# Kernel optimization log

Hardware: AMD Instinct MI355X
Metric: run time of the kernel (lower is better)

The kernel has to match this reference:

```python
import jax, jax.numpy as jnp
import numpy as np

B, T, I, H = 512, 256, 7, 64


def setup_inputs() -> dict:
    key = jax.random.key(0)
    d = {
        "x": jax.random.normal(jax.random.fold_in(key, 0), (B, T, I), jnp.float32),
        "C": jnp.zeros((B, H, H), jnp.float32),
        "n": jnp.zeros((B, H, H), jnp.float32),
    }
    for j, nm in enumerate(["Wq", "Wk", "Wv", "Wi", "Wf", "Wo"]):
        d[nm] = jax.random.normal(jax.random.fold_in(key, j + 1), (H, I), jnp.float32)
        d["b" + nm[1]] = jnp.zeros((H,), jnp.float32)
    return d


def reference(x, C, n, Wq, Wk, Wv, Wi, Wf, Wo, bq, bk, bv, bi, bf, bo):
    # x: [B,T,I]; C,n: [B,H,H] matrix memory / normalizer state
    Hdim = Wq.shape[0]
    scale = 1.0 / jnp.sqrt(jnp.asarray(Hdim, x.dtype))
    q = jnp.einsum('bti,hi->bth', x, Wq) + bq
    k = scale * (jnp.einsum('bti,hi->bth', x, Wk) + bk)
    v = jnp.einsum('bti,hi->bth', x, Wv) + bv
    i = jnp.exp(jnp.einsum('bti,hi->bth', x, Wi) + bi)
    f = jax.nn.sigmoid(jnp.einsum('bti,hi->bth', x, Wf) + bf)
    o = jax.nn.sigmoid(jnp.einsum('bti,hi->bth', x, Wo) + bo)
    # time-major for scan: each gate [T,B,H]
    gates = tuple(jnp.swapaxes(g, 0, 1) for g in (q, k, v, i, f, o))

    def step(carry, g):
        C, n = carry                      # [B,H,H]
        qt, kt, vt, it, ft, ot = g        # [B,H]
        ik = it * kt                      # [B,H]
        # torch: C = f*C + i*outer(v,k)  -> C[r,c] = f[c]*C[r,c] + i[c]*v[r]*k[c]
        C = ft[:, None, :] * C + ik[:, None, :] * vt[:, :, None]
        # torch: n = f*n + i*k (broadcast over rows)
        n = ft[:, None, :] * n + ik[:, None, :]
        num = jnp.einsum('brc,bc->br', C, qt)          # C @ q
        den = jnp.einsum('brc,br->bc', n, qt)          # n.T @ q
        h = ot * jnp.tanh(num / jnp.maximum(den, 1.0))
        return (C, n), h

    (C, n), hs = jax.lax.scan(step, (C, n), gates)
    return jnp.swapaxes(hs, 0, 1), C, n  # h: [B,T,H]
```

## Files before the change

kernel.cpp:

```cpp
#include <hip/hip_runtime.h>
#include <math.h>

#define B_ 512
#define T_ 256
#define I_ 7
#define H_ 64
#define L_ 16
#define NCH_ (T_ / L_)
#define L2E 1.44269504089f
#define GUARD2 (-21.64f)

typedef short bf16x8 __attribute__((ext_vector_type(8)));
typedef short short4v __attribute__((ext_vector_type(4)));
typedef float f32x4 __attribute__((ext_vector_type(4)));

__device__ __forceinline__ unsigned short f2bf(float f) {
  unsigned u = __float_as_uint(f);
  u += 0x7fff + ((u >> 16) & 1);
  return (unsigned short)(u >> 16);
}
__device__ __forceinline__ float bf2f(unsigned short u) {
  return __uint_as_float(((unsigned)u) << 16);
}
__device__ __forceinline__ float ex2(float x) { return __builtin_amdgcn_exp2f(x); }
__device__ __forceinline__ float lg2(float x) { return __builtin_amdgcn_logf(x); }
__device__ __forceinline__ float logsig2(float a2) {
  return (a2 < GUARD2) ? a2 : -lg2(1.f + ex2(-a2));
}
__device__ __forceinline__ float sig2(float a2) {
  return __fdividef(1.f, 1.f + ex2(-a2));
}

#define PACK_V(C) do {                                                        \
  const float* xp_ = xb + (C) * (L_ * I_);                                    \
  unsigned short vv[8];                                                       \
  _Pragma("unroll") for (int tt = 0; tt < 8; ++tt) {                          \
    const int t = th0 + tt;                                                   \
    float vp = bP;                                                            \
    _Pragma("unroll") for (int jj = 0; jj < 7; ++jj)                          \
      vp = fmaf(xp_[t * 7 + jj], wP[jj], vp);                                 \
    vv[tt] = f2bf(vp);                                                        \
  }                                                                           \
  short4v p0 = {(short)vv[0], (short)vv[1], (short)vv[2], (short)vv[3]};      \
  short4v p1 = {(short)vv[4], (short)vv[5], (short)vv[6], (short)vv[7]};      \
  *(short4v*)&sVT[(C) & 1][lane][th0]     = p0;                               \
  *(short4v*)&sVT[(C) & 1][lane][th0 + 4] = p1;                               \
} while (0)

#define PACK_O(C) do {                                                        \
  const float* xp_ = xb + (C) * (L_ * I_);                                    \
  _Pragma("unroll") for (int tt = 0; tt < 8; ++tt) {                          \
    const int t = th0 + tt;                                                   \
    float op = bP;                                                            \
    _Pragma("unroll") for (int jj = 0; jj < 7; ++jj)                          \
      op = fmaf(xp_[t * 7 + jj], wP[jj], op);                                 \
    sOpre[(C) & 1][t][lane] = f2bf(op);                                       \
  }                                                                           \
} while (0)

#define IK_PRE(C) do {                                                        \
  const float* xp_ = xb + (C) * (L_ * I_);                                    \
  _Pragma("unroll") for (int tt = 0; tt < 8; ++tt) {                          \
    const int t = tb + tt;                                                    \
    float xs[7];                                                              \
    _Pragma("unroll") for (int jj = 0; jj < 7; ++jj) xs[jj] = xp_[t * 7 + jj];\
    float ip = bI2, kp = bK;                                                  \
    _Pragma("unroll") for (int jj = 0; jj < 7; ++jj) {                        \
      ip = fmaf(xs[jj], wi2[jj], ip);                                         \
      kp = fmaf(xs[jj], wk[jj], kp);                                          \
    }                                                                         \
    const float ik = ex2(ip) * kp * 0.125f;                                   \
    ik8[tt] = ik;                                                             \
    sIK[(C) & 1][t][lane] = ik;                                               \
  }                                                                           \
} while (0)

#define IK_EXP(C) do {                                                        \
  float cl[16];                                                               \
  _Pragma("unroll") for (int t = 0; t < 16; ++t) cl[t] = sLs[(C) & 1][lane][t]; \
  _Pragma("unroll") for (int t = 1; t < 16; ++t) cl[t] += cl[t - 1];          \
  const float m = cl[7];                                                      \
  const float scl = ex2(cl[15] - m);                                          \
  unsigned short kh[8];                                                       \
  _Pragma("unroll") for (int tt = 0; tt < 8; ++tt) {                          \
    const int t = tb + tt;                                                    \
    const float u = ik8[tt] * ex2(m - cl[t]);                                 \
    sKt[(C) & 1][t][lane] = f2bf(u);                                          \
    kh[tt] = f2bf(u * scl);                                                   \
  }                                                                           \
  short4v p0 = {(short)kh[0], (short)kh[1], (short)kh[2], (short)kh[3]};      \
  short4v p1 = {(short)kh[4], (short)kh[5], (short)kh[6], (short)kh[7]};      \
  *(short4v*)&sKnT[(C) & 1][lane][tb]     = p0;                               \
  *(short4v*)&sKnT[(C) & 1][lane][tb + 4] = p1;                               \
} while (0)

#define F_HALF(C) do {                                                        \
  const float* xp_ = xb + (C) * (L_ * I_);                                    \
  _Pragma("unroll") for (int tt = 0; tt < 8; ++tt) {                          \
    const int t = ftb + tt;                                                   \
    float fp = bF2;                                                           \
    _Pragma("unroll") for (int jj = 0; jj < 7; ++jj)                          \
      fp = fmaf(xp_[t * 7 + jj], wf2[jj], fp);                                \
    sLs[(C) & 1][lane][t] = logsig2(fp);                                      \
  }                                                                           \
} while (0)

#define SCALQ(C) do {                                                         \
  const float* xp_ = xb + (C) * (L_ * I_);                                    \
  float cl[16];                                                               \
  _Pragma("unroll") for (int t = 0; t < 16; ++t) cl[t] = sLs[(C) & 1][lane][t]; \
  _Pragma("unroll") for (int t = 1; t < 16; ++t) cl[t] += cl[t - 1];          \
  sEM[(C) & 1][lane]   = ex2(cl[7]);                                          \
  sFtot[(C) & 1][lane] = ex2(cl[15]);                                         \
  if (lane < 16) {                                                            \
    float Sqv = wqs[7];                                                       \
    _Pragma("unroll") for (int jj = 0; jj < 7; ++jj)                          \
      Sqv = fmaf(xp_[lane * 7 + jj], wqs[jj], Sqv);                           \
    sSq[(C) & 1][lane] = Sqv;                                                 \
  }                                                                           \
  const float m = cl[7];                                                      \
  _Pragma("unroll") for (int t = 0; t < 8; ++t) {                             \
    float qq = bQ;                                                            \
    _Pragma("unroll") for (int jj = 0; jj < 7; ++jj)                          \
      qq = fmaf(xp_[t * 7 + jj], wq[jj], qq);                                 \
    sQt[(C) & 1][t][lane] = f2bf(qq * ex2(cl[t] - m));                        \
  }                                                                           \
} while (0)

#define QDEN(C) do {                                                          \
  const float* xp_ = xb + (C) * (L_ * I_);                                    \
  float ls[16], cl[16];                                                       \
  _Pragma("unroll") for (int t = 0; t < 16; ++t) ls[t] = sLs[(C) & 1][lane][t]; \
  _Pragma("unroll") for (int t = 0; t < 16; ++t) {                            \
    nv = fmaf(ex2(ls[t]), nv, sIK[(C) & 1][t][lane]);                         \
    sDen[(C) & 1][t][lane] = nv;                                              \
  }                                                                           \
  cl[0] = ls[0];                                                              \
  _Pragma("unroll") for (int t = 1; t < 16; ++t) cl[t] = cl[t - 1] + ls[t];   \
  const float m = cl[7];                                                      \
  _Pragma("unroll") for (int t = 8; t < 16; ++t) {                            \
    float qq = bQ;                                                            \
    _Pragma("unroll") for (int jj = 0; jj < 7; ++jj)                          \
      qq = fmaf(xp_[t * 7 + jj], wq[jj], qq);                                 \
    sQt[(C) & 1][t][lane] = f2bf(qq * ex2(cl[t] - m));                        \
  }                                                                           \
} while (0)

__global__ __launch_bounds__(512, 4) void mlstm_bal(
    const float* __restrict__ x,
    const float* __restrict__ Cin,
    const float* __restrict__ nin,
    const float* __restrict__ Wq, const float* __restrict__ bq,
    const float* __restrict__ Wk, const float* __restrict__ bk,
    const float* __restrict__ Wv, const float* __restrict__ bv,
    const float* __restrict__ Wi, const float* __restrict__ bi,
    const float* __restrict__ Wf, const float* __restrict__ bf,
    const float* __restrict__ Wo, const float* __restrict__ bo,
    float* __restrict__ hout, float* __restrict__ Cout, float* __restrict__ nout)
{
  const int b    = blockIdx.x;
  const int tid  = threadIdx.x;
  const int lane = tid & 63;
  const int w    = __builtin_amdgcn_readfirstlane(tid >> 6);
  const int quad = lane >> 4;
  const int sl   = lane & 15;

  __shared__ __align__(16) unsigned short sQt[2][L_][72];
  __shared__ __align__(16) unsigned short sKt[2][L_][72];
  __shared__ __align__(16) unsigned short sKnT[2][H_][40];
  __shared__ __align__(16) unsigned short sVT[2][H_][40];
  __shared__ __align__(16) unsigned short sS[4][L_][32];
  __shared__ __align__(16) unsigned short sC0[H_][72];
  __shared__ __align__(16) unsigned short sOpre[2][L_][72];
  __shared__ float sDen[2][L_][68];
  __shared__ float sIK[2][L_][H_];
  __shared__ float sLs[2][H_][17];
  __shared__ float sSq[2][L_];
  __shared__ float sEM[2][H_];
  __shared__ float sFtot[2][H_];
  __shared__ float sNv[H_];

  for (int idx = tid; idx < 1024; idx += 512) {
    const int r = idx >> 3, d = idx & 7;
    ((unsigned*)sKnT)[r * 20 + 8 + d] = 0;
    ((unsigned*)sVT)[r * 20 + 8 + d]  = 0;
  }
  for (int idx = tid; idx < 1024; idx += 512) ((unsigned*)sS)[idx] = 0;

  const float* __restrict__ xb = x + (size_t)b * T_ * I_;

  if (w < 4) {
    const int c0  = 16 * w + sl;
    const int th0 = (w < 2) ? 0 : 8;
    float wP[7];
    float bP;
    if ((w & 1) == 0) {
#pragma unroll
      for (int jj = 0; jj < 7; ++jj) wP[jj] = Wv[lane * 7 + jj];
      bP = bv[lane];
    } else {
#pragma unroll
      for (int jj = 0; jj < 7; ++jj) wP[jj] = Wo[lane * 7 + jj] * L2E;
      bP = bo[lane] * L2E;
    }
    f32x4 Cacc[4];
#pragma unroll
    for (int ct = 0; ct < 4; ++ct)
#pragma unroll
      for (int reg = 0; reg < 4; ++reg)
        Cacc[ct][reg] =
            Cin[(size_t)b * H_ * H_ + (size_t)(16 * w + 4 * quad + reg) * H_ + 16 * ct + sl];
    if ((w & 1) == 0) PACK_V(0); else PACK_O(0);
    __syncthreads();
    __syncthreads();
    for (int j = 0; j < NCH_; ++j) {
      const int p = j & 1;
      const bf16x8 aQ0 = *(const bf16x8*)&sQt[p][sl][8 * quad];
      const bf16x8 aQ1 = *(const bf16x8*)&sQt[p][sl][32 + 8 * quad];
      const bf16x8 bK0 = *(const bf16x8*)&sKt[p][sl][8 * quad];
      const bf16x8 bK1 = *(const bf16x8*)&sKt[p][sl][32 + 8 * quad];
      f32x4 Sv = {0.f, 0.f, 0.f, 0.f};
      Sv = __builtin_amdgcn_mfma_f32_16x16x32_bf16(aQ0, bK0, Sv, 0, 0, 0);
      Sv = __builtin_amdgcn_mfma_f32_16x16x32_bf16(aQ1, bK1, Sv, 0, 0, 0);
#pragma unroll
      for (int reg = 0; reg < 4; ++reg) {
        const int t = 4 * quad + reg;
        sS[w][t][sl] = f2bf((sl <= t) ? Sv[reg] : 0.f);
      }
      const bf16x8 aV = *(const bf16x8*)&sVT[p][c0][8 * quad];
#pragma unroll
      for (int ct = 0; ct < 4; ++ct) {
        const int cc = 16 * ct + sl;
        const float em = sEM[p][cc];
        const float ft = sFtot[p][cc];
#pragma unroll
        for (int reg = 0; reg < 4; ++reg)
          sC0[16 * w + 4 * quad + reg][cc] = f2bf(Cacc[ct][reg] * em);
        Cacc[ct] *= ft;
        const bf16x8 bH = *(const bf16x8*)&sKnT[p][cc][8 * quad];
        Cacc[ct] = __builtin_amdgcn_mfma_f32_16x16x32_bf16(aV, bH, Cacc[ct], 0, 0, 0);
      }
      if (j + 1 < NCH_) { if ((w & 1) == 0) PACK_V(j + 1); else PACK_O(j + 1); }
      __syncthreads();
      const bf16x8 bC0a = *(const bf16x8*)&sC0[c0][8 * quad];
      const bf16x8 bC0b = *(const bf16x8*)&sC0[c0][32 + 8 * quad];
      const bf16x8 aS   = *(const bf16x8*)&sS[w][sl][8 * quad];
      f32x4 Num = {0.f, 0.f, 0.f, 0.f};
      Num = __builtin_amdgcn_mfma_f32_16x16x32_bf16(aQ0, bC0a, Num, 0, 0, 0);
      Num = __builtin_amdgcn_mfma_f32_16x16x32_bf16(aQ1, bC0b, Num, 0, 0, 0);
      Num = __builtin_amdgcn_mfma_f32_16x16x32_bf16(aS, aV, Num, 0, 0, 0);
#pragma unroll
      for (int reg = 0; reg < 4; ++reg) {
        const int t = 4 * quad + reg;
        const float den = sDen[p][t][c0];
        const float idn = __fdividef(1.f, fmaxf(den * sSq[p][t], 1.f));
        const float o   = sig2(bf2f(sOpre[p][t][c0]));
        const float y = Num[reg] * idn;
        const float e = ex2(y * 2.88539008178f);
        const float th = 1.f - __fdividef(2.f, e + 1.f);
        hout[(size_t)b * T_ * H_ + (size_t)(j * L_ + t) * H_ + c0] = o * th;
      }
      __syncthreads();
    }
#pragma unroll
    for (int ct = 0; ct < 4; ++ct)
#pragma unroll
      for (int reg = 0; reg < 4; ++reg)
        Cout[(size_t)b * H_ * H_ + (size_t)(16 * w + 4 * quad + reg) * H_ + 16 * ct + sl] =
            Cacc[ct][reg];
  } else if (w == 4 || w == 5) {
    const int tb = (w == 4) ? 0 : 8;
    float wi2[7], wk[7];
#pragma unroll
    for (int jj = 0; jj < 7; ++jj) {
      wi2[jj] = Wi[lane * 7 + jj] * L2E;
      wk[jj]  = Wk[lane * 7 + jj];
    }
    const float bI2 = bi[lane] * L2E, bK = bk[lane];
    float ik8[8];
    IK_PRE(0);
    __syncthreads();
    IK_EXP(0);
    __syncthreads();
    for (int j = 0; j < NCH_; ++j) {
      if (j + 1 < NCH_) IK_PRE(j + 1);
      __syncthreads();
      if (j + 1 < NCH_) IK_EXP(j + 1);
      __syncthreads();
    }
  } else if (w == 6) {
    const int ftb = 0;
    float wf2[7], wq[7], wqs[8];
#pragma unroll
    for (int jj = 0; jj < 7; ++jj) {
      wf2[jj] = Wf[lane * 7 + jj] * L2E;
      wq[jj]  = Wq[lane * 7 + jj];
    }
    const float bF2 = bf[lane] * L2E, bQ = bq[lane];
#pragma unroll
    for (int jj = 0; jj < 7; ++jj) {
      float s = wq[jj];
#pragma unroll
      for (int off = 32; off >= 1; off >>= 1) s += __shfl_xor(s, off);
      wqs[jj] = s;
    }
    {
      float s = bQ;
#pragma unroll
      for (int off = 32; off >= 1; off >>= 1) s += __shfl_xor(s, off);
      wqs[7] = s;
    }
    F_HALF(0);
    __syncthreads();
    SCALQ(0);
    __syncthreads();
    for (int j = 0; j < NCH_; ++j) {
      if (j + 1 < NCH_) F_HALF(j + 1);
      __syncthreads();
      if (j + 1 < NCH_) SCALQ(j + 1);
      __syncthreads();
    }
  } else {
    const int ftb = 8;
    float wf2[7], wq[7];
#pragma unroll
    for (int jj = 0; jj < 7; ++jj) {
      wf2[jj] = Wf[lane * 7 + jj] * L2E;
      wq[jj]  = Wq[lane * 7 + jj];
    }
    const float bF2 = bf[lane] * L2E, bQ = bq[lane];
    float nv = nin[(size_t)b * H_ * H_ + lane];
    F_HALF(0);
    __syncthreads();
    QDEN(0);
    __syncthreads();
    for (int j = 0; j < NCH_; ++j) {
      if (j + 1 < NCH_) F_HALF(j + 1);
      __syncthreads();
      if (j + 1 < NCH_) QDEN(j + 1);
      __syncthreads();
    }
    sNv[lane] = nv;
  }

  __syncthreads();
  {
    const float nvv = sNv[lane];
#pragma unroll
    for (int k = 0; k < 8; ++k)
      nout[(size_t)b * H_ * H_ + (size_t)(8 * w + k) * H_ + lane] = nvv;
  }
}

extern "C" void kernel_launch(void* const* d_in, const int* in_sizes, int n_in,
                              void* d_out, int out_size, void* d_ws, size_t ws_size,
                              hipStream_t stream) {
  const float* xp  = (const float*)d_in[0];
  const float* Cp  = (const float*)d_in[1];
  const float* np_ = (const float*)d_in[2];

  const float* W[6];
  const float* Bv[6];
  if (n_in >= 15 && in_sizes[4] == 64) {
    for (int g = 0; g < 6; ++g) {
      W[g]  = (const float*)d_in[3 + 2 * g];
      Bv[g] = (const float*)d_in[4 + 2 * g];
    }
  } else {
    for (int g = 0; g < 6; ++g) {
      W[g]  = (const float*)d_in[3 + g];
      Bv[g] = (const float*)d_in[9 + g];
    }
  }

  float* hout = (float*)d_out;
  float* Cout = hout + (size_t)B_ * T_ * H_;
  float* nout = Cout + (size_t)B_ * H_ * H_;

  mlstm_bal<<<dim3(B_), dim3(512), 0, stream>>>(
      xp, Cp, np_,
      W[0], Bv[0], W[1], Bv[1], W[2], Bv[2],
      W[3], Bv[3], W[4], Bv[4], W[5], Bv[5],
      hout, Cout, nout);
}
```

Before: 145.6 us.

## Double chunk length to 32 and redistribute gate and denominator work across waves

Chunk length grows from 16 to 32 timesteps, which halves the number of chunk iterations and block-wide barriers. The normalizer recurrence moves into the four compute waves, and the output gate is now computed inline from x instead of being staged in shared memory. Log-forget and i*k values are stored as bf16 to save LDS. The trade-off is more per-wave serial work (a 32-step nv recurrence in each compute wave), extra precision loss from bf16 cumulative log-sums, and heavier unrolled register use.

```diff
diff --git a/kernel.cpp b/kernel.cpp
--- a/kernel.cpp
+++ b/kernel.cpp
@@ -5,8 +5,8 @@
 #define T_ 256
 #define I_ 7
 #define H_ 64
-#define L_ 16
-#define NCH_ (T_ / L_)
+#define LC_ 32
+#define NC_ (T_ / LC_)
 #define L2E 1.44269504089f
 #define GUARD2 (-21.64f)
 
@@ -31,36 +31,25 @@
   return __fdividef(1.f, 1.f + ex2(-a2));
 }
 
-#define PACK_V(C) do {                                                        \
-  const float* xp_ = xb + (C) * (L_ * I_);                                    \
+#define PACK_V32(C) do {                                                      \
+  const float* xp_ = xb + (C) * (LC_ * I_);                                   \
   unsigned short vv[8];                                                       \
   _Pragma("unroll") for (int tt = 0; tt < 8; ++tt) {                          \
-    const int t = th0 + tt;                                                   \
-    float vp = bP;                                                            \
-    _Pragma("unroll") for (int jj = 0; jj < 7; ++jj)                          \
-      vp = fmaf(xp_[t * 7 + jj], wP[jj], vp);                                 \
+    const int t = vt0 + tt;                                                   \
+    float vp = bV;                                                            \
+    _Pragma("unroll") for (int jj = 0; jj < 7; ++jj)                          \
+      vp = fmaf(xp_[t * 7 + jj], wVl[jj], vp);                                \
     vv[tt] = f2bf(vp);                                                        \
   }                                                                           \
   short4v p0 = {(short)vv[0], (short)vv[1], (short)vv[2], (short)vv[3]};      \
   short4v p1 = {(short)vv[4], (short)vv[5], (short)vv[6], (short)vv[7]};      \
-  *(short4v*)&sVT[(C) & 1][lane][th0]     = p0;                               \
-  *(short4v*)&sVT[(C) & 1][lane][th0 + 4] = p1;                               \
-} while (0)
-
-#define PACK_O(C) do {                                                        \
-  const float* xp_ = xb + (C) * (L_ * I_);                                    \
-  _Pragma("unroll") for (int tt = 0; tt < 8; ++tt) {                          \
-    const int t = th0 + tt;                                                   \
-    float op = bP;                                                            \
-    _Pragma("unroll") for (int jj = 0; jj < 7; ++jj)                          \
-      op = fmaf(xp_[t * 7 + jj], wP[jj], op);                                 \
-    sOpre[(C) & 1][t][lane] = f2bf(op);                                       \
-  }                                                                           \
-} while (0)
-
-#define IK_PRE(C) do {                                                        \
-  const float* xp_ = xb + (C) * (L_ * I_);                                    \
-  _Pragma("unroll") for (int tt = 0; tt < 8; ++tt) {                          \
+  *(short4v*)&sVT[(C) & 1][lane][vt0]     = p0;                               \
+  *(short4v*)&sVT[(C) & 1][lane][vt0 + 4] = p1;                               \
+} while (0)
+
+#define IK_PRE32(C) do {                                                      \
+  const float* xp_ = xb + (C) * (LC_ * I_);                                   \
+  _Pragma("unroll") for (int tt = 0; tt < 16; ++tt) {                         \
     const int t = tb + tt;                                                    \
     float xs[7];                                                              \
     _Pragma("unroll") for (int jj = 0; jj < 7; ++jj) xs[jj] = xp_[t * 7 + jj];\
@@ -69,84 +58,82 @@
       ip = fmaf(xs[jj], wi2[jj], ip);                                         \
       kp = fmaf(xs[jj], wk[jj], kp);                                          \
     }                                                                         \
-    const float ik = ex2(ip) * kp * 0.125f;                                   \
-    ik8[tt] = ik;                                                             \
-    sIK[(C) & 1][t][lane] = ik;                                               \
-  }                                                                           \
-} while (0)
-
-#define IK_EXP(C) do {                                                        \
-  float cl[16];                                                               \
-  _Pragma("unroll") for (int t = 0; t < 16; ++t) cl[t] = sLs[(C) & 1][lane][t]; \
-  _Pragma("unroll") for (int t = 1; t < 16; ++t) cl[t] += cl[t - 1];          \
-  const float m = cl[7];                                                      \
-  const float scl = ex2(cl[15] - m);                                          \
-  unsigned short kh[8];                                                       \
-  _Pragma("unroll") for (int tt = 0; tt < 8; ++tt) {                          \
+    sIK[(C) & 1][t][lane] = f2bf(ex2(ip) * kp * 0.125f);                      \
+  }                                                                           \
+} while (0)
+
+#define IK_EXP32(C) do {                                                      \
+  float cl[32];                                                               \
+  _Pragma("unroll") for (int t = 0; t < 32; ++t)                              \
+    cl[t] = bf2f(sLs[(C) & 1][t][lane]);                                      \
+  _Pragma("unroll") for (int t = 1; t < 32; ++t) cl[t] += cl[t - 1];          \
+  const float m = cl[15];                                                     \
+  const float scl = ex2(cl[31] - m);                                          \
+  unsigned short kh[16];                                                      \
+  _Pragma("unroll") for (int tt = 0; tt < 16; ++tt) {                         \
     const int t = tb + tt;                                                    \
-    const float u = ik8[tt] * ex2(m - cl[t]);                                 \
+    const float ik = bf2f(sIK[(C) & 1][t][lane]);                             \
+    const float u = ik * ex2(m - cl[t]);                                      \
     sKt[(C) & 1][t][lane] = f2bf(u);                                          \
     kh[tt] = f2bf(u * scl);                                                   \
   }                                                                           \
-  short4v p0 = {(short)kh[0], (short)kh[1], (short)kh[2], (short)kh[3]};      \
-  short4v p1 = {(short)kh[4], (short)kh[5], (short)kh[6], (short)kh[7]};      \
-  *(short4v*)&sKnT[(C) & 1][lane][tb]     = p0;                               \
-  *(short4v*)&sKnT[(C) & 1][lane][tb + 4] = p1;                               \
-} while (0)
-
-#define F_HALF(C) do {                                                        \
-  const float* xp_ = xb + (C) * (L_ * I_);                                    \
-  _Pragma("unroll") for (int tt = 0; tt < 8; ++tt) {                          \
+  _Pragma("unroll") for (int g = 0; g < 4; ++g) {                             \
+    short4v pk = {(short)kh[4 * g], (short)kh[4 * g + 1],                     \
+                  (short)kh[4 * g + 2], (short)kh[4 * g + 3]};                \
+    *(short4v*)&sKnT[(C) & 1][lane][tb + 4 * g] = pk;                         \
+  }                                                                           \
+} while (0)
+
+#define F_HALF32(C) do {                                                      \
+  const float* xp_ = xb + (C) * (LC_ * I_);                                   \
+  _Pragma("unroll") for (int tt = 0; tt < 16; ++tt) {                         \
     const int t = ftb + tt;                                                   \
     float fp = bF2;                                                           \
     _Pragma("unroll") for (int jj = 0; jj < 7; ++jj)                          \
       fp = fmaf(xp_[t * 7 + jj], wf2[jj], fp);                                \
-    sLs[(C) & 1][lane][t] = logsig2(fp);                                      \
-  }                                                                           \
-} while (0)
-
-#define SCALQ(C) do {                                                         \
-  const float* xp_ = xb + (C) * (L_ * I_);                                    \
-  float cl[16];                                                               \
-  _Pragma("unroll") for (int t = 0; t < 16; ++t) cl[t] = sLs[(C) & 1][lane][t]; \
-  _Pragma("unroll") for (int t = 1; t < 16; ++t) cl[t] += cl[t - 1];          \
-  sEM[(C) & 1][lane]   = ex2(cl[7]);                                          \
-  sFtot[(C) & 1][lane] = ex2(cl[15]);                                         \
-  if (lane < 16) {                                                            \
+    sLs[(C) & 1][t][lane] = f2bf(logsig2(fp));                                \
+  }                                                                           \
+} while (0)
+
+#define SCALQ32(C) do {                                                       \
+  const float* xp_ = xb + (C) * (LC_ * I_);                                   \
+  float cl[32];                                                               \
+  _Pragma("unroll") for (int t = 0; t < 32; ++t)                              \
+    cl[t] = bf2f(sLs[(C) & 1][t][lane]);                                      \
+  _Pragma("unroll") for (int t = 1; t < 32; ++t) cl[t] += cl[t - 1];          \
+  const float m = cl[15];                                                     \
+  sEM[(C) & 1][lane]   = ex2(m);                                              \
+  sFtot[(C) & 1][lane] = ex2(cl[31]);                                         \
+  _Pragma("unroll") for (int t = 0; t < 16; ++t) {                            \
+    float qq = bQ;                                                            \
+    _Pragma("unroll") for (int jj = 0; jj < 7; ++jj)                          \
+      qq = fmaf(xp_[t * 7 + jj], wq[jj], qq);                                 \
+    sQt[(C) & 1][t][lane] = f2bf(qq * ex2(cl[t] - m));                        \
+  }                                                                           \
+} while (0)
+
+#define SQQ32(C) do {                                                         \
+  const float* xp_ = xb + (C) * (LC_ * I_);                                   \
+  float cl[32];                                                               \
+  _Pragma("unroll") for (int t = 0; t < 32; ++t)                              \
+    cl[t] = bf2f(sLs[(C) & 1][t][lane]);                                      \
+  _Pragma("unroll") for (int t = 1; t < 32; ++t) cl[t] += cl[t - 1];          \
+  const float m = cl[15];                                                     \
+  _Pragma("unroll") for (int t = 16; t < 32; ++t) {                           \
+    float qq = bQ;                                                            \
+    _Pragma("unroll") for (int jj = 0; jj < 7; ++jj)                          \
+      qq = fmaf(xp_[t * 7 + jj], wq[jj], qq);                                 \
+    sQt[(C) & 1][t][lane] = f2bf(qq * ex2(cl[t] - m));                        \
+  }                                                                           \
+  if (lane < 32) {                                                            \
     float Sqv = wqs[7];                                                       \
     _Pragma("unroll") for (int jj = 0; jj < 7; ++jj)                          \
       Sqv = fmaf(xp_[lane * 7 + jj], wqs[jj], Sqv);                           \
     sSq[(C) & 1][lane] = Sqv;                                                 \
   }                                                                           \
-  const float m = cl[7];                                                      \
-  _Pragma("unroll") for (int t = 0; t < 8; ++t) {                             \
-    float qq = bQ;                                                            \
-    _Pragma("unroll") for (int jj = 0; jj < 7; ++jj)                          \
-      qq = fmaf(xp_[t * 7 + jj], wq[jj], qq);                                 \
-    sQt[(C) & 1][t][lane] = f2bf(qq * ex2(cl[t] - m));                        \
-  }                                                                           \
-} while (0)
-
-#define QDEN(C) do {                                                          \
-  const float* xp_ = xb + (C) * (L_ * I_);                                    \
-  float ls[16], cl[16];                                                       \
-  _Pragma("unroll") for (int t = 0; t < 16; ++t) ls[t] = sLs[(C) & 1][lane][t]; \
-  _Pragma("unroll") for (int t = 0; t < 16; ++t) {                            \
-    nv = fmaf(ex2(ls[t]), nv, sIK[(C) & 1][t][lane]);                         \
-    sDen[(C) & 1][t][lane] = nv;                                              \
-  }                                                                           \
-  cl[0] = ls[0];                                                              \
-  _Pragma("unroll") for (int t = 1; t < 16; ++t) cl[t] = cl[t - 1] + ls[t];   \
-  const float m = cl[7];                                                      \
-  _Pragma("unroll") for (int t = 8; t < 16; ++t) {                            \
-    float qq = bQ;                                                            \
-    _Pragma("unroll") for (int jj = 0; jj < 7; ++jj)                          \
-      qq = fmaf(xp_[t * 7 + jj], wq[jj], qq);                                 \
-    sQt[(C) & 1][t][lane] = f2bf(qq * ex2(cl[t] - m));                        \
-  }                                                                           \
-} while (0)
-
-__global__ __launch_bounds__(512, 4) void mlstm_bal(
+} while (0)
+
+__global__ __launch_bounds__(512, 4) void mlstm32(
     const float* __restrict__ x,
     const float* __restrict__ Cin,
     const float* __restrict__ nin,
@@ -165,44 +152,33 @@
   const int quad = lane >> 4;
   const int sl   = lane & 15;
 
-  __shared__ __align__(16) unsigned short sQt[2][L_][72];
-  __shared__ __align__(16) unsigned short sKt[2][L_][72];
+  __shared__ __align__(16) unsigned short sQt[2][LC_][72];
+  __shared__ __align__(16) unsigned short sKt[2][LC_][72];
   __shared__ __align__(16) unsigned short sKnT[2][H_][40];
   __shared__ __align__(16) unsigned short sVT[2][H_][40];
-  __shared__ __align__(16) unsigned short sS[4][L_][32];
+  __shared__ __align__(16) unsigned short sS[LC_][40];
   __shared__ __align__(16) unsigned short sC0[H_][72];
-  __shared__ __align__(16) unsigned short sOpre[2][L_][72];
-  __shared__ float sDen[2][L_][68];
-  __shared__ float sIK[2][L_][H_];
-  __shared__ float sLs[2][H_][17];
-  __shared__ float sSq[2][L_];
+  __shared__ unsigned short sLs[2][LC_][66];
+  __shared__ unsigned short sIK[2][LC_][66];
+  __shared__ float sSq[2][LC_];
   __shared__ float sEM[2][H_];
   __shared__ float sFtot[2][H_];
   __shared__ float sNv[H_];
 
-  for (int idx = tid; idx < 1024; idx += 512) {
-    const int r = idx >> 3, d = idx & 7;
-    ((unsigned*)sKnT)[r * 20 + 8 + d] = 0;
-    ((unsigned*)sVT)[r * 20 + 8 + d]  = 0;
-  }
-  for (int idx = tid; idx < 1024; idx += 512) ((unsigned*)sS)[idx] = 0;
+  for (int idx = tid; idx < 640; idx += 512) ((unsigned*)sS)[idx] = 0;
 
   const float* __restrict__ xb = x + (size_t)b * T_ * I_;
 
   if (w < 4) {
     const int c0  = 16 * w + sl;
-    const int th0 = (w < 2) ? 0 : 8;
-    float wP[7];
-    float bP;
-    if ((w & 1) == 0) {
-#pragma unroll
-      for (int jj = 0; jj < 7; ++jj) wP[jj] = Wv[lane * 7 + jj];
-      bP = bv[lane];
-    } else {
-#pragma unroll
-      for (int jj = 0; jj < 7; ++jj) wP[jj] = Wo[lane * 7 + jj] * L2E;
-      bP = bo[lane] * L2E;
-    }
+    const int vt0 = 8 * w;
+    float wOl[7], wVl[7];
+#pragma unroll
+    for (int jj = 0; jj < 7; ++jj) {
+      wOl[jj] = Wo[c0 * 7 + jj] * L2E;
+      wVl[jj] = Wv[lane * 7 + jj];
+    }
+    const float bO2 = bo[c0] * L2E, bV = bv[lane];
     f32x4 Cacc[4];
 #pragma unroll
     for (int ct = 0; ct < 4; ++ct)
@@ -210,22 +186,36 @@
       for (int reg = 0; reg < 4; ++reg)
         Cacc[ct][reg] =
             Cin[(size_t)b * H_ * H_ + (size_t)(16 * w + 4 * quad + reg) * H_ + 16 * ct + sl];
-    if ((w & 1) == 0) PACK_V(0); else PACK_O(0);
-    __syncthreads();
-    __syncthreads();
-    for (int j = 0; j < NCH_; ++j) {
+    float nv = nin[(size_t)b * H_ * H_ + c0];
+    PACK_V32(0);
+    __syncthreads();
+    __syncthreads();
+    for (int j = 0; j < NC_; ++j) {
       const int p = j & 1;
-      const bf16x8 aQ0 = *(const bf16x8*)&sQt[p][sl][8 * quad];
-      const bf16x8 aQ1 = *(const bf16x8*)&sQt[p][sl][32 + 8 * quad];
-      const bf16x8 bK0 = *(const bf16x8*)&sKt[p][sl][8 * quad];
-      const bf16x8 bK1 = *(const bf16x8*)&sKt[p][sl][32 + 8 * quad];
-      f32x4 Sv = {0.f, 0.f, 0.f, 0.f};
-      Sv = __builtin_amdgcn_mfma_f32_16x16x32_bf16(aQ0, bK0, Sv, 0, 0, 0);
-      Sv = __builtin_amdgcn_mfma_f32_16x16x32_bf16(aQ1, bK1, Sv, 0, 0, 0);
-#pragma unroll
-      for (int reg = 0; reg < 4; ++reg) {
-        const int t = 4 * quad + reg;
-        sS[w][t][sl] = f2bf((sl <= t) ? Sv[reg] : 0.f);
+      const float* xc = xb + (size_t)j * LC_ * I_;
+      float den8[8];
+#pragma unroll
+      for (int t = 0; t < 32; ++t) {
+        const float fs = ex2(bf2f(sLs[p][t][c0]));
+        const float ik = bf2f(sIK[p][t][c0]);
+        nv = fmaf(fs, nv, ik);
+        if (((t >> 2) & 3) == quad) den8[((t >> 4) << 2) | (t & 3)] = nv;
+      }
+      if (w != 1) {
+        const int tt = w >> 1, ss2 = w & 1;
+        const bf16x8 aQ0 = *(const bf16x8*)&sQt[p][16 * tt + sl][8 * quad];
+        const bf16x8 aQ1 = *(const bf16x8*)&sQt[p][16 * tt + sl][32 + 8 * quad];
+        const bf16x8 bK0 = *(const bf16x8*)&sKt[p][16 * ss2 + sl][8 * quad];
+        const bf16x8 bK1 = *(const bf16x8*)&sKt[p][16 * ss2 + sl][32 + 8 * quad];
+        f32x4 Sv = {0.f, 0.f, 0.f, 0.f};
+        Sv = __builtin_amdgcn_mfma_f32_16x16x32_bf16(aQ0, bK0, Sv, 0, 0, 0);
+        Sv = __builtin_amdgcn_mfma_f32_16x16x32_bf16(aQ1, bK1, Sv, 0, 0, 0);
+#pragma unroll
+        for (int reg = 0; reg < 4; ++reg) {
+          const int t = 16 * tt + 4 * quad + reg;
+          const int s = 16 * ss2 + sl;
+          sS[t][s] = f2bf((s <= t) ? Sv[reg] : 0.f);
+        }
       }
       const bf16x8 aV = *(const bf16x8*)&sVT[p][c0][8 * quad];
 #pragma unroll
@@ -237,28 +227,36 @@
         for (int reg = 0; reg < 4; ++reg)
           sC0[16 * w + 4 * quad + reg][cc] = f2bf(Cacc[ct][reg] * em);
         Cacc[ct] *= ft;
-        const bf16x8 bH = *(const bf16x8*)&sKnT[p][cc][8 * quad];
-        Cacc[ct] = __builtin_amdgcn_mfma_f32_16x16x32_bf16(aV, bH, Cacc[ct], 0, 0, 0);
+        const bf16x8 bKn = *(const bf16x8*)&sKnT[p][cc][8 * quad];
+        Cacc[ct] = __builtin_amdgcn_mfma_f32_16x16x32_bf16(aV, bKn, Cacc[ct], 0, 0, 0);
       }
-      if (j + 1 < NCH_) { if ((w & 1) == 0) PACK_V(j + 1); else PACK_O(j + 1); }
+      if (j + 1 < NC_) PACK_V32(j + 1);
       __syncthreads();
       const bf16x8 bC0a = *(const bf16x8*)&sC0[c0][8 * quad];
       const bf16x8 bC0b = *(const bf16x8*)&sC0[c0][32 + 8 * quad];
-      const bf16x8 aS   = *(const bf16x8*)&sS[w][sl][8 * quad];
-      f32x4 Num = {0.f, 0.f, 0.f, 0.f};
-      Num = __builtin_amdgcn_mfma_f32_16x16x32_bf16(aQ0, bC0a, Num, 0, 0, 0);
-      Num = __builtin_amdgcn_mfma_f32_16x16x32_bf16(aQ1, bC0b, Num, 0, 0, 0);
-      Num = __builtin_amdgcn_mfma_f32_16x16x32_bf16(aS, aV, Num, 0, 0, 0);
-#pragma unroll
-      for (int reg = 0; reg < 4; ++reg) {
-        const int t = 4 * quad + reg;
-        const float den = sDen[p][t][c0];
-        const float idn = __fdividef(1.f, fmaxf(den * sSq[p][t], 1.f));
-        const float o   = sig2(bf2f(sOpre[p][t][c0]));
-        const float y = Num[reg] * idn;
-        const float e = ex2(y * 2.88539008178f);
-        const float th = 1.f - __fdividef(2.f, e + 1.f);
-        hout[(size_t)b * T_ * H_ + (size_t)(j * L_ + t) * H_ + c0] = o * th;
+#pragma unroll
+      for (int tt = 0; tt < 2; ++tt) {
+        const bf16x8 aQ0 = *(const bf16x8*)&sQt[p][16 * tt + sl][8 * quad];
+        const bf16x8 aQ1 = *(const bf16x8*)&sQt[p][16 * tt + sl][32 + 8 * quad];
+        const bf16x8 aS  = *(const bf16x8*)&sS[16 * tt + sl][8 * quad];
+        f32x4 Num = {0.f, 0.f, 0.f, 0.f};
+        Num = __builtin_amdgcn_mfma_f32_16x16x32_bf16(aQ0, bC0a, Num, 0, 0, 0);
+        Num = __builtin_amdgcn_mfma_f32_16x16x32_bf16(aQ1, bC0b, Num, 0, 0, 0);
+        Num = __builtin_amdgcn_mfma_f32_16x16x32_bf16(aS, aV, Num, 0, 0, 0);
+#pragma unroll
+        for (int reg = 0; reg < 4; ++reg) {
+          const int t = 16 * tt + 4 * quad + reg;
+          const float den = den8[tt * 4 + reg];
+          const float idn = __fdividef(1.f, fmaxf(den * sSq[p][t], 1.f));
+          float op = bO2;
+#pragma unroll
+          for (int jj = 0; jj < 7; ++jj) op = fmaf(xc[t * 7 + jj], wOl[jj], op);
+          const float o = sig2(op);
+          const float y = Num[reg] * idn;
+          const float e = ex2(y * 2.88539008178f);
+          const float th = 1.f - __fdividef(2.f, e + 1.f);
+          hout[(size_t)b * T_ * H_ + (size_t)(j * LC_ + t) * H_ + c0] = o * th;
+        }
       }
       __syncthreads();
     }
@@ -268,8 +266,9 @@
       for (int reg = 0; reg < 4; ++reg)
         Cout[(size_t)b * H_ * H_ + (size_t)(16 * w + 4 * quad + reg) * H_ + 16 * ct + sl] =
             Cacc[ct][reg];
+    if (quad == 0) sNv[c0] = nv;
   } else if (w == 4 || w == 5) {
-    const int tb = (w == 4) ? 0 : 8;
+    const int tb = (w == 4) ? 0 : 16;
     float wi2[7], wk[7];
 #pragma unroll
     for (int jj = 0; jj < 7; ++jj) {
@@ -277,26 +276,44 @@
       wk[jj]  = Wk[lane * 7 + jj];
     }
     const float bI2 = bi[lane] * L2E, bK = bk[lane];
-    float ik8[8];
-    IK_PRE(0);
-    __syncthreads();
-    IK_EXP(0);
-    __syncthreads();
-    for (int j = 0; j < NCH_; ++j) {
-      if (j + 1 < NCH_) IK_PRE(j + 1);
-      __syncthreads();
-      if (j + 1 < NCH_) IK_EXP(j + 1);
+    IK_PRE32(0);
+    __syncthreads();
+    IK_EXP32(0);
+    __syncthreads();
+    for (int j = 0; j < NC_; ++j) {
+      if (j + 1 < NC_) IK_PRE32(j + 1);
+      __syncthreads();
+      if (j + 1 < NC_) IK_EXP32(j + 1);
       __syncthreads();
     }
   } else if (w == 6) {
     const int ftb = 0;
-    float wf2[7], wq[7], wqs[8];
+    float wf2[7], wq[7];
 #pragma unroll
     for (int jj = 0; jj < 7; ++jj) {
       wf2[jj] = Wf[lane * 7 + jj] * L2E;
       wq[jj]  = Wq[lane * 7 + jj];
     }
     const float bF2 = bf[lane] * L2E, bQ = bq[lane];
+    F_HALF32(0);
+    __syncthreads();
+    SCALQ32(0);
+    __syncthreads();
+    for (int j = 0; j < NC_; ++j) {
+      if (j + 1 < NC_) F_HALF32(j + 1);
+      __syncthreads();
+      if (j + 1 < NC_) SCALQ32(j + 1);
+      __syncthreads();
+    }
+  } else {
+    const int ftb = 16;
+    float wf2[7], wq[7], wqs[8];
+#pragma unroll
+    for (int jj = 0; jj < 7; ++jj) {
+      wf2[jj] = Wf[lane * 7 + jj] * L2E;
+      wq[jj]  = Wq[lane * 7 + jj];
+    }
+    const float bF2 = bf[lane] * L2E, bQ = bq[lane];
 #pragma unroll
     for (int jj = 0; jj < 7; ++jj) {
       float s = wq[jj];
@@ -310,37 +327,16 @@
       for (int off = 32; off >= 1; off >>= 1) s += __shfl_xor(s, off);
       wqs[7] = s;
     }
-    F_HALF(0);
-    __syncthreads();
-    SCALQ(0);
-    __syncthreads();
-    for (int j = 0; j < NCH_; ++j) {
-      if (j + 1 < NCH_) F_HALF(j + 1);
-      __syncthreads();
-      if (j + 1 < NCH_) SCALQ(j + 1);
-      __syncthreads();
-    }
-  } else {
-    const int ftb = 8;
-    float wf2[7], wq[7];
-#pragma unroll
-    for (int jj = 0; jj < 7; ++jj) {
-      wf2[jj] = Wf[lane * 7 + jj] * L2E;
-      wq[jj]  = Wq[lane * 7 + jj];
-    }
-    const float bF2 = bf[lane] * L2E, bQ = bq[lane];
-    float nv = nin[(size_t)b * H_ * H_ + lane];
-    F_HALF(0);
-    __syncthreads();
-    QDEN(0);
-    __syncthreads();
-    for (int j = 0; j < NCH_; ++j) {
-      if (j + 1 < NCH_) F_HALF(j + 1);
-      __syncthreads();
-      if (j + 1 < NCH_) QDEN(j + 1);
-      __syncthreads();
-    }
-    sNv[lane] = nv;
+    F_HALF32(0);
+    __syncthreads();
+    SQQ32(0);
+    __syncthreads();
+    for (int j = 0; j < NC_; ++j) {
+      if (j + 1 < NC_) F_HALF32(j + 1);
+      __syncthreads();
+      if (j + 1 < NC_) SQQ32(j + 1);
+      __syncthreads();
+    }
   }
 
   __syncthreads();
@@ -377,7 +373,7 @@
   float* Cout = hout + (size_t)B_ * T_ * H_;
   float* nout = Cout + (size_t)B_ * H_ * H_;
 
-  mlstm_bal<<<dim3(B_), dim3(512), 0, stream>>>(
+  mlstm32<<<dim3(B_), dim3(512), 0, stream>>>(
       xp, Cp, np_,
       W[0], Bv[0], W[1], Bv[1], W[2], Bv[2],
       W[3], Bv[3], W[4], Bv[4], W[5], Bv[5],
```

Measured after the change: 168.0 us. +15.5%, slower.

## Offload V and O gate packing from MFMA waves to four dedicated waves

Applied to the files above, without the earlier changes.

The block grows from 8 to 12 waves. The V-gate and O-gate projection and packing, previously done by the four MFMA waves between their matrix-update and output phases, now run on four extra producer waves (two for V, two for O). This takes the packing work off the critical MFMA waves, so it overlaps with the recurrent C update and output computation. The cost is more threads per block, which may lower occupancy and register budget under the new launch bounds. Barrier counts are kept matched, with the V and O producer waves placing their pack calls at different barrier phases.

```diff
diff --git a/kernel.cpp b/kernel.cpp
--- a/kernel.cpp
+++ b/kernel.cpp
@@ -146,7 +146,7 @@
   }                                                                           \
 } while (0)
 
-__global__ __launch_bounds__(512, 4) void mlstm_bal(
+__global__ __launch_bounds__(768, 6) void mlstm_w12(
     const float* __restrict__ x,
     const float* __restrict__ Cin,
     const float* __restrict__ nin,
@@ -180,29 +180,17 @@
   __shared__ float sFtot[2][H_];
   __shared__ float sNv[H_];
 
-  for (int idx = tid; idx < 1024; idx += 512) {
+  for (int idx = tid; idx < 1024; idx += 768) {
     const int r = idx >> 3, d = idx & 7;
     ((unsigned*)sKnT)[r * 20 + 8 + d] = 0;
     ((unsigned*)sVT)[r * 20 + 8 + d]  = 0;
   }
-  for (int idx = tid; idx < 1024; idx += 512) ((unsigned*)sS)[idx] = 0;
+  for (int idx = tid; idx < 1024; idx += 768) ((unsigned*)sS)[idx] = 0;
 
   const float* __restrict__ xb = x + (size_t)b * T_ * I_;
 
   if (w < 4) {
-    const int c0  = 16 * w + sl;
-    const int th0 = (w < 2) ? 0 : 8;
-    float wP[7];
-    float bP;
-    if ((w & 1) == 0) {
-#pragma unroll
-      for (int jj = 0; jj < 7; ++jj) wP[jj] = Wv[lane * 7 + jj];
-      bP = bv[lane];
-    } else {
-#pragma unroll
-      for (int jj = 0; jj < 7; ++jj) wP[jj] = Wo[lane * 7 + jj] * L2E;
-      bP = bo[lane] * L2E;
-    }
+    const int c0 = 16 * w + sl;
     f32x4 Cacc[4];
 #pragma unroll
     for (int ct = 0; ct < 4; ++ct)
@@ -210,7 +198,6 @@
       for (int reg = 0; reg < 4; ++reg)
         Cacc[ct][reg] =
             Cin[(size_t)b * H_ * H_ + (size_t)(16 * w + 4 * quad + reg) * H_ + 16 * ct + sl];
-    if ((w & 1) == 0) PACK_V(0); else PACK_O(0);
     __syncthreads();
     __syncthreads();
     for (int j = 0; j < NCH_; ++j) {
@@ -240,7 +227,6 @@
         const bf16x8 bH = *(const bf16x8*)&sKnT[p][cc][8 * quad];
         Cacc[ct] = __builtin_amdgcn_mfma_f32_16x16x32_bf16(aV, bH, Cacc[ct], 0, 0, 0);
       }
-      if (j + 1 < NCH_) { if ((w & 1) == 0) PACK_V(j + 1); else PACK_O(j + 1); }
       __syncthreads();
       const bf16x8 bC0a = *(const bf16x8*)&sC0[c0][8 * quad];
       const bf16x8 bC0b = *(const bf16x8*)&sC0[c0][32 + 8 * quad];
@@ -320,7 +306,7 @@
       if (j + 1 < NCH_) SCALQ(j + 1);
       __syncthreads();
     }
-  } else {
+  } else if (w == 7) {
     const int ftb = 8;
     float wf2[7], wq[7];
 #pragma unroll
@@ -341,10 +327,38 @@
       __syncthreads();
     }
     sNv[lane] = nv;
+  } else if (w == 8 || w == 9) {
+    const int th0 = (w == 8) ? 0 : 8;
+    float wP[7];
+#pragma unroll
+    for (int jj = 0; jj < 7; ++jj) wP[jj] = Wv[lane * 7 + jj];
+    const float bP = bv[lane];
+    PACK_V(0);
+    __syncthreads();
+    __syncthreads();
+    for (int j = 0; j < NCH_; ++j) {
+      if (j + 1 < NCH_) PACK_V(j + 1);
+      __syncthreads();
+      __syncthreads();
+    }
+  } else {
+    const int th0 = (w == 10) ? 0 : 8;
+    float wP[7];
+#pragma unroll
+    for (int jj = 0; jj < 7; ++jj) wP[jj] = Wo[lane * 7 + jj] * L2E;
+    const float bP = bo[lane] * L2E;
+    PACK_O(0);
+    __syncthreads();
+    __syncthreads();
+    for (int j = 0; j < NCH_; ++j) {
+      __syncthreads();
+      if (j + 1 < NCH_) PACK_O(j + 1);
+      __syncthreads();
+    }
   }
 
   __syncthreads();
-  {
+  if (w < 8) {
     const float nvv = sNv[lane];
 #pragma unroll
     for (int k = 0; k < 8; ++k)
@@ -377,7 +391,7 @@
   float* Cout = hout + (size_t)B_ * T_ * H_;
   float* nout = Cout + (size_t)B_ * H_ * H_;
 
-  mlstm_bal<<<dim3(B_), dim3(512), 0, stream>>>(
+  mlstm_w12<<<dim3(B_), dim3(768), 0, stream>>>(
       xp, Cp, np_,
       W[0], Bv[0], W[1], Bv[1], W[2], Bv[2],
       W[3], Bv[3], W[4], Bv[4], W[5], Bv[5],
```

New measurement: 141.7 us. 1.03x faster.
